# Optimization experiments

Measured on AMD Instinct MI355X. Metric: run time of the kernel, lower is better.

Reference implementation:

```python
import jax, jax.numpy as jnp
import numpy as np

EPS = 1e-5

def _layernorm(x, w, b):
    mu = jnp.mean(x, axis=-1, keepdims=True)
    var = jnp.mean(jnp.square(x - mu), axis=-1, keepdims=True)
    return (x - mu) * jax.lax.rsqrt(var + EPS) * w + b

def setup_inputs() -> dict:
    key = jax.random.key(0)
    ks = jax.random.split(key, 6)
    B, Np, Nc, D, P = 2, 512, 512, 128, 128
    p_embed = jax.random.normal(ks[0], (B, Np, D), dtype=jnp.float32)
    c_embed = jax.random.normal(ks[1], (B, Nc, D), dtype=jnp.float32)
    p_mask = jnp.ones((B, Np), dtype=bool)
    c_mask = jnp.ones((B, Nc), dtype=bool)
    ln_p_w = jnp.ones((D,), jnp.float32)
    ln_p_b = jnp.zeros((D,), jnp.float32)
    ln_c_w = jnp.ones((D,), jnp.float32)
    ln_c_b = jnp.zeros((D,), jnp.float32)
    W_out = jax.random.normal(ks[2], (P, D), dtype=jnp.float32) / np.sqrt(D)
    b_out = jax.random.normal(ks[3], (P,), dtype=jnp.float32) * 0.01
    return {"p_embed": p_embed, "c_embed": c_embed, "p_mask": p_mask,
            "c_mask": c_mask, "ln_p_w": ln_p_w, "ln_p_b": ln_p_b,
            "ln_c_w": ln_c_w, "ln_c_b": ln_c_b, "W_out": W_out, "b_out": b_out}

def reference(p_embed, c_embed, p_mask, c_mask, ln_p_w, ln_p_b, ln_c_w, ln_c_b, W_out, b_out):
    # inter_mask[b,i,j] = p_mask[b,i] & c_mask[b,j]
    inter_mask = p_mask[..., :, None] & c_mask[..., None, :]
    p = _layernorm(p_embed, ln_p_w, ln_p_b)  # [B,Np,D]
    c = _layernorm(c_embed, ln_c_w, ln_c_b)  # [B,Nc,D]
    # einsum '...ik,...jk->...ijk' followed by Linear(D->P), fused into one
    # contraction so the [B,Np,Nc,D] intermediate is never materialized:
    # out[b,i,j,h] = sum_k p[b,i,k]*c[b,j,k]*W_out[h,k] + b_out[h]
    inter = jnp.einsum('bik,bjk,hk->bijh', p, c, W_out) + b_out
    inter = inter * inter_mask[..., None].astype(inter.dtype)
    return inter, inter_mask
```

## Files before the change

kernel.cpp:

```cpp
#include <hip/hip_runtime.h>
#include <hip/hip_bf16.h>

#define BATCH 2
#define NP 512
#define NC 512
#define DD 128
#define PP 128

typedef __bf16 bf16_t;
typedef __bf16 bf16x8 __attribute__((ext_vector_type(8)));
typedef float f32x4 __attribute__((ext_vector_type(4)));

__global__ __launch_bounds__(64) void ln_kernel(const float* __restrict__ x,
                                                const float* __restrict__ w,
                                                const float* __restrict__ bsh,
                                                float* __restrict__ y) {
    int row = blockIdx.x;
    int t = threadIdx.x;
    const float* xr = x + (size_t)row * DD;
    float2 v = *(const float2*)&xr[2 * t];
    float s  = v.x + v.y;
    float sq = v.x * v.x + v.y * v.y;
    for (int o = 32; o; o >>= 1) {
        s  += __shfl_xor(s, o);
        sq += __shfl_xor(sq, o);
    }
    float mu  = s * (1.0f / 128.0f);
    float var = sq * (1.0f / 128.0f) - mu * mu;
    float rs  = rsqrtf(var + 1e-5f);
    float2 wv = *(const float2*)&w[2 * t];
    float2 bv = *(const float2*)&bsh[2 * t];
    float* yr = y + (size_t)row * DD;
    float2 o2;
    o2.x = (v.x - mu) * rs * wv.x + bv.x;
    o2.y = (v.y - mu) * rs * wv.y + bv.y;
    *(float2*)&yr[2 * t] = o2;
}

__global__ __launch_bounds__(256) void cvt_kernel(const float* __restrict__ W,
                                                  bf16_t* __restrict__ Wb) {
    int idx = blockIdx.x * 256 + threadIdx.x;
    Wb[idx] = (bf16_t)W[idx];
}

__global__ __launch_bounds__(256) void inter_kernel(
    const float* __restrict__ p_ln, const float* __restrict__ c_ln,
    const bf16_t* __restrict__ Wb, const float* __restrict__ b_out,
    const int* __restrict__ p_mask,
    const int* __restrict__ c_mask,
    float* __restrict__ out) {
    __shared__ bf16_t As[128][136];
    __shared__ bf16_t Ws[128][136];

    int blk = blockIdx.x;
    int jt = blk & 3;
    int i  = (blk >> 2) & 511;
    int b  = blk >> 11;
    int j0 = jt * 128;

    int t = threadIdx.x;
    int kcol = (t & 15) * 8;
    int rgrp = t >> 4;

    const float* prow = p_ln + ((size_t)(b * NP + i)) * DD + kcol;
    float4 p0 = *(const float4*)&prow[0];
    float4 p1 = *(const float4*)&prow[4];

    const float* cbase = c_ln + ((size_t)(b * NC + j0)) * DD;
    #pragma unroll
    for (int pass = 0; pass < 8; ++pass) {
        int row = pass * 16 + rgrp;
        const float* cr = cbase + (size_t)row * DD + kcol;
        float4 c0 = *(const float4*)&cr[0];
        float4 c1 = *(const float4*)&cr[4];
        bf16x8 av;
        av[0] = (bf16_t)(c0.x * p0.x); av[1] = (bf16_t)(c0.y * p0.y);
        av[2] = (bf16_t)(c0.z * p0.z); av[3] = (bf16_t)(c0.w * p0.w);
        av[4] = (bf16_t)(c1.x * p1.x); av[5] = (bf16_t)(c1.y * p1.y);
        av[6] = (bf16_t)(c1.z * p1.z); av[7] = (bf16_t)(c1.w * p1.w);
        *(bf16x8*)&As[row][kcol] = av;
        const bf16_t* wr = Wb + (size_t)row * DD + kcol;
        *(bf16x8*)&Ws[row][kcol] = *(const bf16x8*)wr;
    }
    __syncthreads();

    int lane = t & 63;
    int wave = t >> 6;
    int wm = wave >> 1, wn = wave & 1;
    int m0 = wm * 64, n0 = wn * 64;
    int l16 = lane & 15, q = lane >> 4;

    f32x4 acc[4][4];
    #pragma unroll
    for (int mi = 0; mi < 4; ++mi)
        #pragma unroll
        for (int ni = 0; ni < 4; ++ni)
            acc[mi][ni] = (f32x4){0.f, 0.f, 0.f, 0.f};

    #pragma unroll
    for (int kk = 0; kk < 4; ++kk) {
        int kb = kk * 32 + q * 8;
        bf16x8 a[4], w[4];
        #pragma unroll
        for (int mi = 0; mi < 4; ++mi)
            a[mi] = *(const bf16x8*)&As[m0 + mi * 16 + l16][kb];
        #pragma unroll
        for (int ni = 0; ni < 4; ++ni)
            w[ni] = *(const bf16x8*)&Ws[n0 + ni * 16 + l16][kb];
        #pragma unroll
        for (int mi = 0; mi < 4; ++mi)
            #pragma unroll
            for (int ni = 0; ni < 4; ++ni)
                acc[mi][ni] = __builtin_amdgcn_mfma_f32_16x16x32_bf16(
                    a[mi], w[ni], acc[mi][ni], 0, 0, 0);
    }

    int pm = p_mask[b * NP + i];
    float bias[4];
    #pragma unroll
    for (int ni = 0; ni < 4; ++ni)
        bias[ni] = b_out[n0 + ni * 16 + l16];

    size_t outbase = (((size_t)b * NP + i) * NC) * PP;
    #pragma unroll
    for (int mi = 0; mi < 4; ++mi) {
        #pragma unroll
        for (int reg = 0; reg < 4; ++reg) {
            int j = j0 + m0 + mi * 16 + q * 4 + reg;
            int cm = c_mask[b * NC + j];
            float scale = (pm != 0 && cm != 0) ? 1.0f : 0.0f;
            float* orow = out + outbase + (size_t)j * PP;
            #pragma unroll
            for (int ni = 0; ni < 4; ++ni)
                orow[n0 + ni * 16 + l16] = (acc[mi][ni][reg] + bias[ni]) * scale;
        }
    }

    if (t < 128) {
        int j = j0 + t;
        int cm = c_mask[b * NC + j];
        size_t mbase = (size_t)BATCH * NP * NC * PP;
        out[mbase + ((size_t)b * NP + i) * NC + j] =
            (pm != 0 && cm != 0) ? 1.0f : 0.0f;
    }
}

extern "C" void kernel_launch(void* const* d_in, const int* in_sizes, int n_in,
                              void* d_out, int out_size, void* d_ws, size_t ws_size,
                              hipStream_t stream) {
    const float* p_embed = (const float*)d_in[0];
    const float* c_embed = (const float*)d_in[1];
    const int* p_mask = (const int*)d_in[2];
    const int* c_mask = (const int*)d_in[3];
    const float* ln_p_w = (const float*)d_in[4];
    const float* ln_p_b = (const float*)d_in[5];
    const float* ln_c_w = (const float*)d_in[6];
    const float* ln_c_b = (const float*)d_in[7];
    const float* W_out  = (const float*)d_in[8];
    const float* b_out  = (const float*)d_in[9];
    float* out = (float*)d_out;

    float* p_ln = (float*)d_ws;
    float* c_ln = p_ln + (size_t)BATCH * NP * DD;
    bf16_t* w_bf = (bf16_t*)(c_ln + (size_t)BATCH * NC * DD);

    ln_kernel<<<BATCH * NP, 64, 0, stream>>>(p_embed, ln_p_w, ln_p_b, p_ln);
    ln_kernel<<<BATCH * NC, 64, 0, stream>>>(c_embed, ln_c_w, ln_c_b, c_ln);
    cvt_kernel<<<(PP * DD) / 256, 256, 0, stream>>>(W_out, w_bf);
    inter_kernel<<<BATCH * NP * (NC / 128), 256, 0, stream>>>(
        p_ln, c_ln, w_bf, b_out, p_mask, c_mask, out);
}
```

Before: 284.7 us.

## Fold p row into W fragments, stream bf16 c rows without shared memory

Refactors the contraction so each block handles one p row: it scales W by p once into register-resident bf16 fragments and then streams all 512 c rows from global memory as bf16. This drops the shared-memory staging, the barrier and the per-block rebuild of the p*c product, and stores the output as f32x4 vectors. The two LayerNorm launches are merged into one, and c is written directly in bf16, which removes the separate W conversion kernel. In exchange the grid shrinks to 1024 blocks and each block loops sequentially over 32 j tiles. Rounding also shifts, since bf16 is now applied to c and to W*p rather than to p*c and W.

```diff
diff --git a/kernel.cpp b/kernel.cpp
--- a/kernel.cpp
+++ b/kernel.cpp
@@ -9,16 +9,22 @@
 
 typedef __bf16 bf16_t;
 typedef __bf16 bf16x8 __attribute__((ext_vector_type(8)));
+typedef __bf16 bf16x2 __attribute__((ext_vector_type(2)));
 typedef float f32x4 __attribute__((ext_vector_type(4)));
 
-__global__ __launch_bounds__(64) void ln_kernel(const float* __restrict__ x,
-                                                const float* __restrict__ w,
-                                                const float* __restrict__ bsh,
-                                                float* __restrict__ y) {
+__global__ __launch_bounds__(64) void ln_kernel(
+    const float* __restrict__ p, const float* __restrict__ c,
+    const float* __restrict__ pw, const float* __restrict__ pb,
+    const float* __restrict__ cw, const float* __restrict__ cb,
+    float* __restrict__ p_ln, bf16_t* __restrict__ c_bf) {
     int row = blockIdx.x;
+    bool isP = row < BATCH * NP;
+    int crow = row - BATCH * NP;
+    const float* x  = isP ? p + (size_t)row * DD : c + (size_t)crow * DD;
+    const float* w  = isP ? pw : cw;
+    const float* bs = isP ? pb : cb;
     int t = threadIdx.x;
-    const float* xr = x + (size_t)row * DD;
-    float2 v = *(const float2*)&xr[2 * t];
+    float2 v = *(const float2*)&x[2 * t];
     float s  = v.x + v.y;
     float sq = v.x * v.x + v.y * v.y;
     for (int o = 32; o; o >>= 1) {
@@ -29,119 +35,87 @@
     float var = sq * (1.0f / 128.0f) - mu * mu;
     float rs  = rsqrtf(var + 1e-5f);
     float2 wv = *(const float2*)&w[2 * t];
-    float2 bv = *(const float2*)&bsh[2 * t];
-    float* yr = y + (size_t)row * DD;
-    float2 o2;
-    o2.x = (v.x - mu) * rs * wv.x + bv.x;
-    o2.y = (v.y - mu) * rs * wv.y + bv.y;
-    *(float2*)&yr[2 * t] = o2;
+    float2 bv = *(const float2*)&bs[2 * t];
+    float o0 = (v.x - mu) * rs * wv.x + bv.x;
+    float o1 = (v.y - mu) * rs * wv.y + bv.y;
+    if (isP) {
+        float2 o2; o2.x = o0; o2.y = o1;
+        *(float2*)&p_ln[(size_t)row * DD + 2 * t] = o2;
+    } else {
+        bf16x2 o2; o2[0] = (bf16_t)o0; o2[1] = (bf16_t)o1;
+        *(bf16x2*)&c_bf[(size_t)crow * DD + 2 * t] = o2;
+    }
 }
 
-__global__ __launch_bounds__(256) void cvt_kernel(const float* __restrict__ W,
-                                                  bf16_t* __restrict__ Wb) {
-    int idx = blockIdx.x * 256 + threadIdx.x;
-    Wb[idx] = (bf16_t)W[idx];
-}
-
-__global__ __launch_bounds__(256) void inter_kernel(
-    const float* __restrict__ p_ln, const float* __restrict__ c_ln,
-    const bf16_t* __restrict__ Wb, const float* __restrict__ b_out,
+__global__ __launch_bounds__(256, 4) void inter_kernel(
+    const float* __restrict__ p_ln, const bf16_t* __restrict__ c_bf,
+    const float* __restrict__ W, const float* __restrict__ b_out,
     const int* __restrict__ p_mask,
     const int* __restrict__ c_mask,
     float* __restrict__ out) {
-    __shared__ bf16_t As[128][136];
-    __shared__ bf16_t Ws[128][136];
-
     int blk = blockIdx.x;
-    int jt = blk & 3;
-    int i  = (blk >> 2) & 511;
-    int b  = blk >> 11;
-    int j0 = jt * 128;
-
+    int i = blk & (NP - 1);
+    int b = blk >> 9;
     int t = threadIdx.x;
-    int kcol = (t & 15) * 8;
-    int rgrp = t >> 4;
-
-    const float* prow = p_ln + ((size_t)(b * NP + i)) * DD + kcol;
-    float4 p0 = *(const float4*)&prow[0];
-    float4 p1 = *(const float4*)&prow[4];
-
-    const float* cbase = c_ln + ((size_t)(b * NC + j0)) * DD;
-    #pragma unroll
-    for (int pass = 0; pass < 8; ++pass) {
-        int row = pass * 16 + rgrp;
-        const float* cr = cbase + (size_t)row * DD + kcol;
-        float4 c0 = *(const float4*)&cr[0];
-        float4 c1 = *(const float4*)&cr[4];
-        bf16x8 av;
-        av[0] = (bf16_t)(c0.x * p0.x); av[1] = (bf16_t)(c0.y * p0.y);
-        av[2] = (bf16_t)(c0.z * p0.z); av[3] = (bf16_t)(c0.w * p0.w);
-        av[4] = (bf16_t)(c1.x * p1.x); av[5] = (bf16_t)(c1.y * p1.y);
-        av[6] = (bf16_t)(c1.z * p1.z); av[7] = (bf16_t)(c1.w * p1.w);
-        *(bf16x8*)&As[row][kcol] = av;
-        const bf16_t* wr = Wb + (size_t)row * DD + kcol;
-        *(bf16x8*)&Ws[row][kcol] = *(const bf16x8*)wr;
-    }
-    __syncthreads();
-
     int lane = t & 63;
     int wave = t >> 6;
-    int wm = wave >> 1, wn = wave & 1;
-    int m0 = wm * 64, n0 = wn * 64;
     int l16 = lane & 15, q = lane >> 4;
 
-    f32x4 acc[4][4];
+    int pm = p_mask[b * NP + i];
+
+    const float* pr = p_ln + ((size_t)(b * NP + i)) * DD;
+    bf16x8 wf[2][4];
     #pragma unroll
-    for (int mi = 0; mi < 4; ++mi)
+    for (int ht = 0; ht < 2; ++ht) {
+        int h = wave * 32 + ht * 16 + l16;
+        const float* wr = W + (size_t)h * DD;
         #pragma unroll
-        for (int ni = 0; ni < 4; ++ni)
-            acc[mi][ni] = (f32x4){0.f, 0.f, 0.f, 0.f};
-
-    #pragma unroll
-    for (int kk = 0; kk < 4; ++kk) {
-        int kb = kk * 32 + q * 8;
-        bf16x8 a[4], w[4];
-        #pragma unroll
-        for (int mi = 0; mi < 4; ++mi)
-            a[mi] = *(const bf16x8*)&As[m0 + mi * 16 + l16][kb];
-        #pragma unroll
-        for (int ni = 0; ni < 4; ++ni)
-            w[ni] = *(const bf16x8*)&Ws[n0 + ni * 16 + l16][kb];
-        #pragma unroll
-        for (int mi = 0; mi < 4; ++mi)
-            #pragma unroll
-            for (int ni = 0; ni < 4; ++ni)
-                acc[mi][ni] = __builtin_amdgcn_mfma_f32_16x16x32_bf16(
-                    a[mi], w[ni], acc[mi][ni], 0, 0, 0);
-    }
-
-    int pm = p_mask[b * NP + i];
-    float bias[4];
-    #pragma unroll
-    for (int ni = 0; ni < 4; ++ni)
-        bias[ni] = b_out[n0 + ni * 16 + l16];
-
-    size_t outbase = (((size_t)b * NP + i) * NC) * PP;
-    #pragma unroll
-    for (int mi = 0; mi < 4; ++mi) {
-        #pragma unroll
-        for (int reg = 0; reg < 4; ++reg) {
-            int j = j0 + m0 + mi * 16 + q * 4 + reg;
-            int cm = c_mask[b * NC + j];
-            float scale = (pm != 0 && cm != 0) ? 1.0f : 0.0f;
-            float* orow = out + outbase + (size_t)j * PP;
-            #pragma unroll
-            for (int ni = 0; ni < 4; ++ni)
-                orow[n0 + ni * 16 + l16] = (acc[mi][ni][reg] + bias[ni]) * scale;
+        for (int kt = 0; kt < 4; ++kt) {
+            int k = kt * 32 + q * 8;
+            float4 w0 = *(const float4*)&wr[k];
+            float4 w1 = *(const float4*)&wr[k + 4];
+            float4 pv0 = *(const float4*)&pr[k];
+            float4 pv1 = *(const float4*)&pr[k + 4];
+            bf16x8 f;
+            f[0] = (bf16_t)(w0.x * pv0.x); f[1] = (bf16_t)(w0.y * pv0.y);
+            f[2] = (bf16_t)(w0.z * pv0.z); f[3] = (bf16_t)(w0.w * pv0.w);
+            f[4] = (bf16_t)(w1.x * pv1.x); f[5] = (bf16_t)(w1.y * pv1.y);
+            f[6] = (bf16_t)(w1.z * pv1.z); f[7] = (bf16_t)(w1.w * pv1.w);
+            wf[ht][kt] = f;
         }
     }
 
-    if (t < 128) {
-        int j = j0 + t;
-        int cm = c_mask[b * NC + j];
-        size_t mbase = (size_t)BATCH * NP * NC * PP;
-        out[mbase + ((size_t)b * NP + i) * NC + j] =
-            (pm != 0 && cm != 0) ? 1.0f : 0.0f;
+    f32x4 bias0 = *(const f32x4*)&b_out[wave * 32 + q * 4];
+    f32x4 bias1 = *(const f32x4*)&b_out[wave * 32 + 16 + q * 4];
+
+    const bf16_t* cbb = c_bf + (size_t)b * NC * DD;
+    const int* cmb = c_mask + b * NC;
+    size_t outbase = (((size_t)b * NP + i) * NC) * PP;
+
+    #pragma unroll 2
+    for (int jt = 0; jt < NC / 16; ++jt) {
+        int j = jt * 16 + l16;
+        bf16x8 cf[4];
+        #pragma unroll
+        for (int kt = 0; kt < 4; ++kt)
+            cf[kt] = *(const bf16x8*)&cbb[(size_t)j * DD + kt * 32 + q * 8];
+        f32x4 acc0 = {0.f, 0.f, 0.f, 0.f};
+        f32x4 acc1 = {0.f, 0.f, 0.f, 0.f};
+        #pragma unroll
+        for (int kt = 0; kt < 4; ++kt) {
+            acc0 = __builtin_amdgcn_mfma_f32_16x16x32_bf16(wf[0][kt], cf[kt], acc0, 0, 0, 0);
+            acc1 = __builtin_amdgcn_mfma_f32_16x16x32_bf16(wf[1][kt], cf[kt], acc1, 0, 0, 0);
+        }
+        float scale = (pm != 0 && cmb[j] != 0) ? 1.0f : 0.0f;
+        float* orow = out + outbase + (size_t)j * PP + wave * 32 + q * 4;
+        *(f32x4*)&orow[0]  = (acc0 + bias0) * scale;
+        *(f32x4*)&orow[16] = (acc1 + bias1) * scale;
+    }
+
+    size_t mbase = (size_t)BATCH * NP * NC * PP;
+    for (int jj = t; jj < NC; jj += 256) {
+        out[mbase + ((size_t)b * NP + i) * NC + jj] =
+            (pm != 0 && cmb[jj] != 0) ? 1.0f : 0.0f;
     }
 }
 
@@ -161,12 +135,10 @@
     float* out = (float*)d_out;
 
     float* p_ln = (float*)d_ws;
-    float* c_ln = p_ln + (size_t)BATCH * NP * DD;
-    bf16_t* w_bf = (bf16_t*)(c_ln + (size_t)BATCH * NC * DD);
+    bf16_t* c_bf = (bf16_t*)(p_ln + (size_t)BATCH * NP * DD);
 
-    ln_kernel<<<BATCH * NP, 64, 0, stream>>>(p_embed, ln_p_w, ln_p_b, p_ln);
-    ln_kernel<<<BATCH * NC, 64, 0, stream>>>(c_embed, ln_c_w, ln_c_b, c_ln);
-    cvt_kernel<<<(PP * DD) / 256, 256, 0, stream>>>(W_out, w_bf);
-    inter_kernel<<<BATCH * NP * (NC / 128), 256, 0, stream>>>(
-        p_ln, c_ln, w_bf, b_out, p_mask, c_mask, out);
+    ln_kernel<<<BATCH * (NP + NC), 64, 0, stream>>>(
+        p_embed, c_embed, ln_p_w, ln_p_b, ln_c_w, ln_c_b, p_ln, c_bf);
+    inter_kernel<<<BATCH * NP, 256, 0, stream>>>(
+        p_ln, c_bf, W_out, b_out, p_mask, c_mask, out);
 }
```

Result: slower. 316.9 us (+11.3%).
